# Optimization experiments

Measured on AMD Instinct MI355X. Metric: run time of the kernel, lower is better.

Reference implementation:

```python
import jax, jax.numpy as jnp
import numpy as np


def conv1x1(x, w, b):
    # x: [B,C,H,W], w: [O,C], b: [O]
    return jnp.einsum('bchw,oc->bohw', x, w) + b[None, :, None, None]


def dwconv(x, w):
    # depthwise conv, x: [B,C,H,W], w: [C,1,k,k], SAME padding (k odd, pad=k//2)
    return jax.lax.conv_general_dilated(
        x, w, window_strides=(1, 1), padding='SAME',
        dimension_numbers=('NCHW', 'OIHW', 'NCHW'),
        feature_group_count=x.shape[1])


def setup_inputs() -> dict:
    key = jax.random.key(0)
    ks = jax.random.split(key, 14)
    B, C, H, W = 16, 256, 64, 64
    OC = C // 16  # scale=16 -> 16
    WSCALE = 0.05
    r = lambda k, shape: jax.random.normal(k, shape, dtype=jnp.float32) * WSCALE
    return {
        'x': jax.random.normal(ks[0], (B, C, H, W), dtype=jnp.float32),
        'conv_w': r(ks[1], (C + 4, C)),           # 1x1 conv -> ctx (C) + gates (3+1)
        'conv_b': r(ks[2], (C + 4,)),
        'fw3': r(ks[3], (C, 1, 3, 3)),            # depthwise focal kernels
        'fw5': r(ks[4], (C, 1, 5, 5)),
        'fw7': r(ks[5], (C, 1, 7, 7)),
        'key_w': r(ks[6], (1, C)),                # Conv_key 1x1
        'key_b': r(ks[7], (1,)),
        'v1_w': r(ks[8], (OC, C)),                # Conv_value first 1x1
        'v1_b': r(ks[9], (OC,)),
        'ln_w': jnp.ones((OC,), dtype=jnp.float32),
        'ln_b': jnp.zeros((OC,), dtype=jnp.float32),
        'v2_w': r(ks[10], (C, OC)),               # Conv_value second 1x1
        'v2_b': r(ks[11], (C,)),
    }


def reference(x, conv_w, conv_b, fw3, fw5, fw7, key_w, key_b,
              v1_w, v1_b, ln_w, ln_b, v2_w, v2_b):
    B, C, H, W = x.shape
    # _contextAggregation
    t = conv1x1(x, conv_w, conv_b)          # [B, C+4, H, W]
    ctx, gates = t[:, :C], t[:, C:]         # [B,C,H,W], [B,4,H,W]
    ctx_all = jnp.zeros_like(ctx)
    for l, fw in enumerate((fw3, fw5, fw7)):
        ctx = jax.nn.gelu(dwconv(ctx, fw), approximate=False)  # torch GELU = exact erf
        ctx_all = ctx_all + ctx * gates[:, l:l + 1]
    ctx_global = jnp.mean(ctx, axis=(2, 3), keepdims=True)     # AdaptiveAvgPool2d(1)
    ctx_all = ctx_all + ctx_global * gates[:, 3:4]
    # GC-style channel attention: softmax over spatial positions
    k = conv1x1(ctx_all, key_w, key_b).reshape(B, H * W)       # [B, HW]
    k = jax.nn.softmax(k, axis=1)
    q = ctx_all.reshape(B, C, H * W)
    qk = jnp.einsum('bcn,bn->bc', q, k)[:, :, None, None]      # [B,C,1,1]
    # Conv_value: 1x1 -> LayerNorm([OC,1,1]) -> ReLU -> 1x1
    v = conv1x1(qk, v1_w, v1_b)                                # [B,OC,1,1]
    mu = jnp.mean(v, axis=(1, 2, 3), keepdims=True)
    var = jnp.var(v, axis=(1, 2, 3), keepdims=True)
    v = (v - mu) * jax.lax.rsqrt(var + 1e-5)
    v = v * ln_w[None, :, None, None] + ln_b[None, :, None, None]
    v = jax.nn.relu(v)
    v = conv1x1(v, v2_w, v2_b)                                 # [B,C,1,1]
    return ctx_all + v
```

## Files before the change

### kernel.cpp

```cpp
#include <hip/hip_runtime.h>

#define DEVFN __device__ __forceinline__

constexpr int B  = 16;
constexpr int C  = 256;
constexpr int N  = 64 * 64;
constexpr int O1 = C + 4;

typedef __attribute__((ext_vector_type(8)))  short bf16x8;
typedef __attribute__((ext_vector_type(4)))  short bf16x4;
typedef __attribute__((ext_vector_type(16))) float f32x16;
typedef __attribute__((ext_vector_type(2)))  _Float16 h2;
typedef unsigned short ushort_t;
typedef unsigned int   uint32;

DEVFN short f2bf(float f){
  union { float f; unsigned u; } p; p.f = f;
  unsigned r = p.u + 0x7fffu + ((p.u >> 16) & 1u);
  return (short)(r >> 16);
}
DEVFN unsigned pack2(float lo, float hi){
  return (unsigned)(ushort_t)f2bf(lo) | ((unsigned)(ushort_t)f2bf(hi) << 16);
}
DEVFN float lo2f(unsigned u){ union{unsigned u; float f;} p; p.u = u << 16; return p.f; }
DEVFN float hi2f(unsigned u){ union{unsigned u; float f;} p; p.u = u & 0xffff0000u; return p.f; }
DEVFN float bf2f(ushort_t s){ union{unsigned u; float f;} p; p.u = (unsigned)s << 16; return p.f; }

DEVFN float gelu_fast(float x){
  float s = x * x;
  float t = x * fmaf(s, 0.1029432f, 2.3022082f);
  float e = __builtin_amdgcn_exp2f(-t);
  return x * __builtin_amdgcn_rcpf(1.0f + e);
}

DEVFN float fdot2f(uint32 a, uint32 b, float c){
#if __has_builtin(__builtin_amdgcn_fdot2)
  return __builtin_amdgcn_fdot2(__builtin_bit_cast(h2, a),
                                __builtin_bit_cast(h2, b), c, false);
#else
  h2 ha = __builtin_bit_cast(h2, a), hb = __builtin_bit_cast(h2, b);
  return fmaf((float)ha.x, (float)hb.x, fmaf((float)ha.y, (float)hb.y, c));
#endif
}

DEVFN uint32 pkh(float a, float b){
  _Float16 ha = (_Float16)a, hb = (_Float16)b;
  return (uint32)__builtin_bit_cast(ushort_t, ha) |
         ((uint32)__builtin_bit_cast(ushort_t, hb) << 16);
}

__global__ __launch_bounds__(256)
void k_wbf(const float* __restrict__ w, ushort_t* __restrict__ wbf,
           const float* __restrict__ fw3, const float* __restrict__ fw5,
           const float* __restrict__ fw7, uint32* __restrict__ w3p,
           uint32* __restrict__ w5p, uint32* __restrict__ w7p){
  if(blockIdx.x == 320){
    const int c = threadIdx.x;
    #pragma unroll
    for(int ky = 0; ky < 3; ky++){
      const float* wr = fw3 + c * 9 + ky * 3;
      w3p[c * 6 + ky * 2 + 0] = pkh(wr[0], wr[1]);
      w3p[c * 6 + ky * 2 + 1] = pkh(wr[2], 0.f);
    }
    #pragma unroll
    for(int ky = 0; ky < 5; ky++){
      const float* wr = fw5 + c * 25 + ky * 5;
      w5p[c * 15 + ky * 3 + 0] = pkh(wr[0], wr[1]);
      w5p[c * 15 + ky * 3 + 1] = pkh(wr[2], wr[3]);
      w5p[c * 15 + ky * 3 + 2] = pkh(wr[4], 0.f);
    }
    #pragma unroll
    for(int ky = 0; ky < 7; ky++){
      const float* wr = fw7 + c * 49 + ky * 7;
      w7p[c * 28 + ky * 4 + 0] = pkh(wr[0], wr[1]);
      w7p[c * 28 + ky * 4 + 1] = pkh(wr[2], wr[3]);
      w7p[c * 28 + ky * 4 + 2] = pkh(wr[4], wr[5]);
      w7p[c * 28 + ky * 4 + 3] = pkh(wr[6], 0.f);
    }
    return;
  }
  int idx = blockIdx.x * 256 + threadIdx.x;
  int o = idx >> 8, cc = idx & 255;
  wbf[idx] = (o < O1) ? (ushort_t)f2bf(w[o * 256 + cc]) : (ushort_t)0;
}

__global__ __launch_bounds__(256, 3)
void k_conv1_mfma(const float* __restrict__ x, const ushort_t* __restrict__ wbf,
                  const float* __restrict__ bias, ushort_t* __restrict__ ctxb,
                  float* __restrict__ gates){
  __shared__ __align__(16) short wlds[8 * 320 * 8];
  __shared__ __align__(16) short xlds[8 * 64 * 8];
  __shared__ float sbias[320];
  const int tid  = threadIdx.x;
  const int wave = tid >> 6;
  const int lane = tid & 63;
  const int l31  = lane & 31;
  const int lhi  = lane >> 5;
  const int pg0  = blockIdx.x * 64;
  const int b    = pg0 >> 12;
  const int n0   = pg0 & 4095;
  const int nwv  = (wave & 1) * 32;
  const int mrow = wave >> 1;

  sbias[tid] = bias[tid];
  if(tid < 64) sbias[256 + tid] = (256 + tid < O1) ? bias[256 + tid] : 0.f;

  const float* xpb = x + (size_t)b * C * N + n0;

  f32x16 acc[5];
  #pragma unroll
  for(int t = 0; t < 5; t++)
    #pragma unroll
    for(int r = 0; r < 16; r++) acc[t][r] = 0.f;

  float xf[2][8];

  auto pfX = [&](int kc){
    #pragma unroll
    for(int p = 0; p < 2; p++){
      const int idx = p * 256 + tid;
      const int kg = idx >> 6, n = idx & 63;
      const float* xp = xpb + (size_t)(kc + kg * 8) * N + n;
      #pragma unroll
      for(int j = 0; j < 8; j++) xf[p][j] = xp[(size_t)j * N];
    }
  };
  auto stX = [&](){
    #pragma unroll
    for(int p = 0; p < 2; p++){
      const int idx = p * 256 + tid;
      const int kg = idx >> 6, n = idx & 63;
      uint4 v;
      v.x = pack2(xf[p][0], xf[p][1]); v.y = pack2(xf[p][2], xf[p][3]);
      v.z = pack2(xf[p][4], xf[p][5]); v.w = pack2(xf[p][6], xf[p][7]);
      *(uint4*)&xlds[(kg * 64 + n) * 8] = v;
    }
  };
  auto stW = [&](int kc){
    #pragma unroll
    for(int q = 0; q < 10; q++){
      const int pidx = q * 256 + tid;
      const int kg = pidx / 320;
      const int m  = pidx - kg * 320;
      uint4 v = *(const uint4*)(wbf + (size_t)m * 256 + kc + kg * 8);
      *(uint4*)&wlds[(kg * 320 + m) * 8] = v;
    }
  };
  auto mfmaC = [&](){
    #pragma unroll
    for(int ks = 0; ks < 4; ks++){
      const int kg = ks * 2 + lhi;
      bf16x8 bfr = *(const bf16x8*)&xlds[(kg * 64 + nwv + l31) * 8];
      #pragma unroll
      for(int t = 0; t < 5; t++){
        const int m0 = (mrow + 2 * t) * 32;
        bf16x8 af = *(const bf16x8*)&wlds[(kg * 320 + m0 + l31) * 8];
        acc[t] = __builtin_amdgcn_mfma_f32_32x32x16_bf16(af, bfr, acc[t], 0, 0, 0);
      }
    }
  };

  stW(0); pfX(0); stX();
  __syncthreads();
  pfX(64);
  mfmaC();
  __syncthreads();
  stW(64); stX();
  __syncthreads();
  pfX(128);
  mfmaC();
  __syncthreads();
  stW(128); stX();
  __syncthreads();
  pfX(192);
  mfmaC();
  __syncthreads();
  stW(192); stX();
  __syncthreads();
  mfmaC();

  const int n = n0 + nwv + l31;
  #pragma unroll
  for(int t = 0; t < 5; t++){
    const int mt = (mrow + 2 * t) * 32;
    #pragma unroll
    for(int r = 0; r < 16; r++){
      const int row = (r & 3) + 8 * (r >> 2) + 4 * lhi;
      const int o = mt + row;
      if(o >= O1) continue;
      const float v = acc[t][r] + sbias[o];
      if(o < 256){
        _Float16 hv = (_Float16)v;
        ctxb[((size_t)(b * 256 + o)) * N + n] = __builtin_bit_cast(ushort_t, hv);
      } else {
        gates[((size_t)(b * 4 + (o - 256))) * N + n] = v;
      }
    }
  }
}

constexpr int SSTR = 72;

template<int K>
DEVFN void dw_stage_dot(const short* src, const uint32* __restrict__ wp,
                        int h, int w0, float* val){
  constexpr int R = K / 2;
  constexpr int PAIRS = (K + 2) / 2;
  float acc[8];
  #pragma unroll
  for(int i = 0; i < 8; i++) acc[i] = 0.f;
  #pragma unroll
  for(int ky = 0; ky < K; ky++){
    uint32 wk[PAIRS];
    #pragma unroll
    for(int t = 0; t < PAIRS; t++) wk[t] = wp[ky * PAIRS + t];
    const int r = h + ky - R;
    if((unsigned)r < 64u){
      const short* rp = &src[r * SSTR + w0];
      uint4 a0 = *(const uint4*)rp;
      uint4 a1 = *(const uint4*)(rp + 8);
      uint32 P[8] = {a0.x, a0.y, a0.z, a0.w, a1.x, a1.y, a1.z, a1.w};
      uint32 S[7];
      #pragma unroll
      for(int j = 0; j < 7; j++)
        S[j] = __builtin_amdgcn_alignbit(P[j + 1], P[j], 16);
      #pragma unroll
      for(int i = 0; i < 8; i++){
        int j0, useP;
        if      (K == 7){ useP =  (i & 1); j0 = (i + 1) >> 1; }
        else if (K == 5){ useP = !(i & 1); j0 = (i >> 1) + 1; }
        else            { useP =  (i & 1); j0 = (i >> 1) + ((i & 1) ? 2 : 1); }
        #pragma unroll
        for(int t = 0; t < PAIRS; t++){
          const uint32 a = useP ? P[j0 + t] : S[j0 + t];
          acc[i] = fdot2f(a, wk[t], acc[i]);
        }
      }
    }
  }
  #pragma unroll
  for(int i = 0; i < 8; i++) val[i] = gelu_fast(acc[i]);
}

DEVFN void store_row_h(short* dst, int h, int w0, const float* val){
  uint32 o0 = __builtin_bit_cast(uint32, __builtin_amdgcn_cvt_pkrtz(val[0], val[1]));
  uint32 o1 = __builtin_bit_cast(uint32, __builtin_amdgcn_cvt_pkrtz(val[2], val[3]));
  uint32 o2 = __builtin_bit_cast(uint32, __builtin_amdgcn_cvt_pkrtz(val[4], val[5]));
  uint32 o3 = __builtin_bit_cast(uint32, __builtin_amdgcn_cvt_pkrtz(val[6], val[7]));
  uint2 t0; t0.x = o0; t0.y = o1;
  uint2 t1; t1.x = o2; t1.y = o3;
  *(uint2*)&dst[h * SSTR + w0 + 4] = t0;
  *(uint2*)&dst[h * SSTR + w0 + 8] = t1;
}

__global__ __launch_bounds__(512, 8)
void k_dwchain(ushort_t* __restrict__ ctxb, const uint32* __restrict__ w3p,
               const uint32* __restrict__ w5p, const uint32* __restrict__ w7p,
               const float* __restrict__ gates){
  __shared__ __align__(16) short bufA[64 * SSTR];
  __shared__ __align__(16) short bufB[64 * SSTR];
  __shared__ float wred[8];
  const int tid = threadIdx.x;
  const int plane = blockIdx.x;
  const int b = plane >> 8;
  const int c = plane & 255;
  const int h  = tid >> 3;
  const int w0 = (tid & 7) * 8;
  const int nbase = h * 64 + w0;

  if(tid < 64){
    bf16x4 z = {0, 0, 0, 0};
    *(bf16x4*)&bufA[tid * SSTR] = z;  *(bf16x4*)&bufA[tid * SSTR + 68] = z;
    *(bf16x4*)&bufB[tid * SSTR] = z;  *(bf16x4*)&bufB[tid * SSTR + 68] = z;
  }
  {
    const uint4 iv = *(const uint4*)((const short*)ctxb + (size_t)plane * N + tid * 8);
    uint2 t0; t0.x = iv.x; t0.y = iv.y;
    uint2 t1; t1.x = iv.z; t1.y = iv.w;
    *(uint2*)&bufA[h * SSTR + w0 + 4] = t0;
    *(uint2*)&bufA[h * SSTR + w0 + 8] = t1;
  }
  __syncthreads();

  float ctxp[8];
  #pragma unroll
  for(int i = 0; i < 8; i++) ctxp[i] = 0.f;
  float val[8];

  dw_stage_dot<3>(bufA, w3p + c * 6, h, w0, val);
  {
    const float* gp = gates + ((size_t)(b * 4 + 0)) * N + nbase;
    float4 ga = *(const float4*)gp, gb = *(const float4*)(gp + 4);
    ctxp[0] = fmaf(val[0], ga.x, ctxp[0]); ctxp[1] = fmaf(val[1], ga.y, ctxp[1]);
    ctxp[2] = fmaf(val[2], ga.z, ctxp[2]); ctxp[3] = fmaf(val[3], ga.w, ctxp[3]);
    ctxp[4] = fmaf(val[4], gb.x, ctxp[4]); ctxp[5] = fmaf(val[5], gb.y, ctxp[5]);
    ctxp[6] = fmaf(val[6], gb.z, ctxp[6]); ctxp[7] = fmaf(val[7], gb.w, ctxp[7]);
    store_row_h(bufB, h, w0, val);
  }
  __syncthreads();

  dw_stage_dot<5>(bufB, w5p + c * 15, h, w0, val);
  {
    const float* gp = gates + ((size_t)(b * 4 + 1)) * N + nbase;
    float4 ga = *(const float4*)gp, gb = *(const float4*)(gp + 4);
    ctxp[0] = fmaf(val[0], ga.x, ctxp[0]); ctxp[1] = fmaf(val[1], ga.y, ctxp[1]);
    ctxp[2] = fmaf(val[2], ga.z, ctxp[2]); ctxp[3] = fmaf(val[3], ga.w, ctxp[3]);
    ctxp[4] = fmaf(val[4], gb.x, ctxp[4]); ctxp[5] = fmaf(val[5], gb.y, ctxp[5]);
    ctxp[6] = fmaf(val[6], gb.z, ctxp[6]); ctxp[7] = fmaf(val[7], gb.w, ctxp[7]);
    store_row_h(bufA, h, w0, val);
  }
  __syncthreads();

  dw_stage_dot<7>(bufA, w7p + c * 28, h, w0, val);
  float lsum = 0.f;
  {
    const float* gp = gates + ((size_t)(b * 4 + 2)) * N + nbase;
    float4 ga = *(const float4*)gp, gb = *(const float4*)(gp + 4);
    ctxp[0] = fmaf(val[0], ga.x, ctxp[0]); ctxp[1] = fmaf(val[1], ga.y, ctxp[1]);
    ctxp[2] = fmaf(val[2], ga.z, ctxp[2]); ctxp[3] = fmaf(val[3], ga.w, ctxp[3]);
    ctxp[4] = fmaf(val[4], gb.x, ctxp[4]); ctxp[5] = fmaf(val[5], gb.y, ctxp[5]);
    ctxp[6] = fmaf(val[6], gb.z, ctxp[6]); ctxp[7] = fmaf(val[7], gb.w, ctxp[7]);
    #pragma unroll
    for(int i = 0; i < 8; i++) lsum += val[i];
  }
  #pragma unroll
  for(int off = 32; off > 0; off >>= 1) lsum += __shfl_xor(lsum, off, 64);
  if((tid & 63) == 0) wred[tid >> 6] = lsum;
  __syncthreads();
  float mean = 0.f;
  #pragma unroll
  for(int i = 0; i < 8; i++) mean += wred[i];
  mean *= (1.0f / 4096.0f);

  {
    const float* gp = gates + ((size_t)(b * 4 + 3)) * N + nbase;
    float4 ga = *(const float4*)gp, gb = *(const float4*)(gp + 4);
    bf16x8 ov;
    ov[0] = f2bf(fmaf(mean, ga.x, ctxp[0])); ov[1] = f2bf(fmaf(mean, ga.y, ctxp[1]));
    ov[2] = f2bf(fmaf(mean, ga.z, ctxp[2])); ov[3] = f2bf(fmaf(mean, ga.w, ctxp[3]));
    ov[4] = f2bf(fmaf(mean, gb.x, ctxp[4])); ov[5] = f2bf(fmaf(mean, gb.y, ctxp[5]));
    ov[6] = f2bf(fmaf(mean, gb.z, ctxp[6])); ov[7] = f2bf(fmaf(mean, gb.w, ctxp[7]));
    *(bf16x8*)((short*)ctxb + (size_t)plane * N + nbase) = ov;
  }
}

__global__ __launch_bounds__(256)
void k_logits(const ushort_t* __restrict__ P, const float* __restrict__ key_w,
              const float* __restrict__ key_b, float* __restrict__ logits){
  __shared__ float kw[256];
  __shared__ float part[512];
  int tid = threadIdx.x;
  kw[tid] = key_w[tid];
  __syncthreads();
  int b  = blockIdx.x >> 5;
  int n0 = (blockIdx.x & 31) * 128;
  int cpart = tid >> 6, pxp = tid & 63;
  const ushort_t* pp = P + ((size_t)(b * 256 + cpart * 64)) * N + n0 + pxp * 2;
  float a0 = 0.f, a1 = 0.f;
  #pragma unroll 8
  for(int c = 0; c < 64; c++){
    unsigned u = *(const unsigned*)(pp + (size_t)c * N);
    float kwv = kw[cpart * 64 + c];
    a0 = fmaf(lo2f(u), kwv, a0);
    a1 = fmaf(hi2f(u), kwv, a1);
  }
  part[cpart * 128 + pxp * 2]     = a0;
  part[cpart * 128 + pxp * 2 + 1] = a1;
  __syncthreads();
  if(tid < 128){
    float l = part[tid] + part[128 + tid] + part[256 + tid] + part[384 + tid];
    logits[b * N + n0 + tid] = l + key_b[0];
  }
}

__global__ __launch_bounds__(1024)
void k_softmax(float* __restrict__ kbuf){
  __shared__ float wred[16];
  int b = blockIdx.x, tid = threadIdx.x;
  const int wave = tid >> 6, lane = tid & 63;
  float v[4];
  float m = -1e30f;
  #pragma unroll
  for(int i = 0; i < 4; i++){
    v[i] = kbuf[b * N + tid + i * 1024];
    m = fmaxf(m, v[i]);
  }
  #pragma unroll
  for(int off = 32; off > 0; off >>= 1) m = fmaxf(m, __shfl_xor(m, off, 64));
  if(lane == 0) wred[wave] = m;
  __syncthreads();
  float mm = -1e30f;
  #pragma unroll
  for(int i = 0; i < 16; i++) mm = fmaxf(mm, wred[i]);
  __syncthreads();
  float s = 0.f;
  #pragma unroll
  for(int i = 0; i < 4; i++){ v[i] = __expf(v[i] - mm); s += v[i]; }
  #pragma unroll
  for(int off = 32; off > 0; off >>= 1) s += __shfl_xor(s, off, 64);
  if(lane == 0) wred[wave] = s;
  __syncthreads();
  float tot = 0.f;
  #pragma unroll
  for(int i = 0; i < 16; i++) tot += wred[i];
  float inv = 1.0f / tot;
  #pragma unroll
  for(int i = 0; i < 4; i++)
    kbuf[b * N + tid + i * 1024] = v[i] * inv;
}

__global__ __launch_bounds__(256)
void k_qk(const ushort_t* __restrict__ P, const float* __restrict__ kbuf,
          float* __restrict__ qk){
  __shared__ float red[256];
  int plane = blockIdx.x, tid = threadIdx.x;
  int b = plane >> 8;
  const unsigned* pp = (const unsigned*)(P + (size_t)plane * N);
  const float2* kp = (const float2*)(kbuf + b * N);
  float acc = 0.f;
  #pragma unroll
  for(int i = 0; i < 8; i++){
    int idx = tid + i * 256;
    unsigned u = pp[idx];
    float2 kk = kp[idx];
    acc = fmaf(lo2f(u), kk.x, acc);
    acc = fmaf(hi2f(u), kk.y, acc);
  }
  red[tid] = acc; __syncthreads();
  for(int s = 128; s > 0; s >>= 1){
    if(tid < s) red[tid] += red[tid + s];
    __syncthreads();
  }
  if(tid == 0) qk[plane] = red[0];
}

__global__ __launch_bounds__(256)
void k_v(const float* __restrict__ qk, const float* __restrict__ v1w,
         const float* __restrict__ v1b, const float* __restrict__ lnw,
         const float* __restrict__ lnb, const float* __restrict__ v2w,
         const float* __restrict__ v2b, float* __restrict__ vout){
  int b = blockIdx.x, tid = threadIdx.x;
  __shared__ float qs[256];
  __shared__ float part[256];
  __shared__ float v1s[16];
  __shared__ float vr[16];
  __shared__ float stats[2];
  qs[tid] = qk[b * 256 + tid];
  __syncthreads();
  int oc = tid >> 4, ln = tid & 15;
  float p = 0.f;
  #pragma unroll
  for(int j = 0; j < 16; j++){
    int cc = ln + j * 16;
    p = fmaf(v1w[oc * 256 + cc], qs[cc], p);
  }
  part[tid] = p;
  __syncthreads();
  if(tid < 16){
    float s = v1b[tid];
    for(int j = 0; j < 16; j++) s += part[tid * 16 + j];
    v1s[tid] = s;
  }
  __syncthreads();
  if(tid == 0){
    float mu = 0.f;
    for(int i = 0; i < 16; i++) mu += v1s[i];
    mu *= (1.f / 16.f);
    float var = 0.f;
    for(int i = 0; i < 16; i++){ float d = v1s[i] - mu; var += d * d; }
    var *= (1.f / 16.f);
    stats[0] = mu; stats[1] = rsqrtf(var + 1e-5f);
  }
  __syncthreads();
  if(tid < 16){
    float vv = (v1s[tid] - stats[0]) * stats[1] * lnw[tid] + lnb[tid];
    vr[tid] = fmaxf(vv, 0.f);
  }
  __syncthreads();
  float o = v2b[tid];
  #pragma unroll
  for(int j = 0; j < 16; j++) o = fmaf(v2w[tid * 16 + j], vr[j], o);
  vout[b * 256 + tid] = o;
}

__global__ __launch_bounds__(256)
void k_final(float* __restrict__ out, const ushort_t* __restrict__ ctxb,
             const float* __restrict__ vout){
  int idx8 = blockIdx.x * 256 + threadIdx.x;
  int plane = idx8 >> 9;
  int off = (idx8 & 511) * 8;
  bf16x8 v = *(const bf16x8*)((const short*)ctxb + (size_t)plane * N + off);
  float vv = vout[plane];
  float4 o0, o1;
  o0.x = bf2f((ushort_t)v[0]) + vv; o0.y = bf2f((ushort_t)v[1]) + vv;
  o0.z = bf2f((ushort_t)v[2]) + vv; o0.w = bf2f((ushort_t)v[3]) + vv;
  o1.x = bf2f((ushort_t)v[4]) + vv; o1.y = bf2f((ushort_t)v[5]) + vv;
  o1.z = bf2f((ushort_t)v[6]) + vv; o1.w = bf2f((ushort_t)v[7]) + vv;
  float* op = out + (size_t)plane * N + off;
  *(float4*)op = o0;
  *(float4*)(op + 4) = o1;
}

extern "C" void kernel_launch(void* const* d_in, const int* in_sizes, int n_in,
                              void* d_out, int out_size, void* d_ws, size_t ws_size,
                              hipStream_t stream){
  const float* x      = (const float*)d_in[0];
  const float* conv_w = (const float*)d_in[1];
  const float* conv_b = (const float*)d_in[2];
  const float* fw3    = (const float*)d_in[3];
  const float* fw5    = (const float*)d_in[4];
  const float* fw7    = (const float*)d_in[5];
  const float* key_w  = (const float*)d_in[6];
  const float* key_b  = (const float*)d_in[7];
  const float* v1_w   = (const float*)d_in[8];
  const float* v1_b   = (const float*)d_in[9];
  const float* ln_w   = (const float*)d_in[10];
  const float* ln_b   = (const float*)d_in[11];
  const float* v2_w   = (const float*)d_in[12];
  const float* v2_b   = (const float*)d_in[13];
  float* out = (float*)d_out;

  const size_t PL = (size_t)B * C * N;
  char* p = (char*)d_ws;
  ushort_t* ctxb = (ushort_t*)p;  p += PL * sizeof(ushort_t);
  float* gates   = (float*)p;     p += (size_t)B * 4 * N * sizeof(float);
  float* kbuf    = (float*)p;     p += (size_t)B * N * sizeof(float);
  float* qkb     = (float*)p;     p += (size_t)B * C * sizeof(float);
  float* vout    = (float*)p;     p += (size_t)B * C * sizeof(float);
  ushort_t* wbf  = (ushort_t*)p;  p += (size_t)320 * 256 * sizeof(ushort_t);
  uint32* w3p    = (uint32*)p;    p += (size_t)256 * 6 * sizeof(uint32);
  uint32* w5p    = (uint32*)p;    p += (size_t)256 * 15 * sizeof(uint32);
  uint32* w7p    = (uint32*)p;

  k_wbf<<<321, 256, 0, stream>>>(conv_w, wbf, fw3, fw5, fw7, w3p, w5p, w7p);
  k_conv1_mfma<<<1024, 256, 0, stream>>>(x, wbf, conv_b, ctxb, gates);
  k_dwchain<<<B * C, 512, 0, stream>>>(ctxb, w3p, w5p, w7p, gates);
  k_logits<<<512, 256, 0, stream>>>(ctxb, key_w, key_b, kbuf);
  k_softmax<<<B, 1024, 0, stream>>>(kbuf);
  k_qk<<<B * C, 256, 0, stream>>>(ctxb, kbuf, qkb);
  k_v<<<B, 256, 0, stream>>>(qkb, v1_w, v1_b, ln_w, ln_b, v2_w, v2_b, vout);
  k_final<<<8192, 256, 0, stream>>>(out, ctxb, vout);
}
```

Before: 270.8 us.

## Split gate channels out of MFMA conv1x1 and widen block to 512 threads

The 1x1 conv kernel no longer pads the 260 output rows to 320 for MFMA. It computes only the 256 ctx channels with MFMA, and the 4 gate channels are computed by scalar FMAs from the staged x tile and fp32 gate weights held in shared memory. The block grows to 8 waves, each owning 32 output rows by 64 pixels. Weight loads are prefetched into registers before the barrier, overlapping them with compute. This removes about 20% of wasted MFMA work and weight traffic, at the cost of extra scalar ALU and LDS reads for the gates on half the threads, and the launch bounds of 512 threads with 6 blocks may force heavy register limits.

```diff
diff --git a/kernel.cpp b/kernel.cpp
--- a/kernel.cpp
+++ b/kernel.cpp
@@ -84,119 +84,136 @@
   wbf[idx] = (o < O1) ? (ushort_t)f2bf(w[o * 256 + cc]) : (ushort_t)0;
 }
 
-__global__ __launch_bounds__(256, 3)
+__global__ __launch_bounds__(512, 6)
 void k_conv1_mfma(const float* __restrict__ x, const ushort_t* __restrict__ wbf,
-                  const float* __restrict__ bias, ushort_t* __restrict__ ctxb,
-                  float* __restrict__ gates){
-  __shared__ __align__(16) short wlds[8 * 320 * 8];
+                  const float* __restrict__ conv_w, const float* __restrict__ bias,
+                  ushort_t* __restrict__ ctxb, float* __restrict__ gates){
+  __shared__ __align__(16) short wlds[8 * 256 * 8];
   __shared__ __align__(16) short xlds[8 * 64 * 8];
-  __shared__ float sbias[320];
+  __shared__ float sgw[4 * 256];
+  __shared__ float sbias[256];
   const int tid  = threadIdx.x;
   const int wave = tid >> 6;
   const int lane = tid & 63;
   const int l31  = lane & 31;
   const int lhi  = lane >> 5;
-  const int pg0  = blockIdx.x * 64;
-  const int b    = pg0 >> 12;
-  const int n0   = pg0 & 4095;
-  const int nwv  = (wave & 1) * 32;
-  const int mrow = wave >> 1;
-
-  sbias[tid] = bias[tid];
-  if(tid < 64) sbias[256 + tid] = (256 + tid < O1) ? bias[256 + tid] : 0.f;
+  const int pg   = blockIdx.x;
+  const int b    = pg >> 6;
+  const int n0   = (pg & 63) * 64;
+
+  #pragma unroll
+  for(int i = 0; i < 2; i++) sgw[i * 512 + tid] = conv_w[256 * 256 + i * 512 + tid];
+  if(tid < 256) sbias[tid] = bias[tid];
+  const int gidx = tid >> 6;
+  const int gn   = tid & 63;
+  float gbias = (tid < 256) ? bias[256 + gidx] : 0.f;
+  float gacc = 0.f;
 
   const float* xpb = x + (size_t)b * C * N + n0;
 
-  f32x16 acc[5];
-  #pragma unroll
-  for(int t = 0; t < 5; t++)
+  f32x16 acc[2];
+  #pragma unroll
+  for(int t = 0; t < 2; t++)
     #pragma unroll
     for(int r = 0; r < 16; r++) acc[t][r] = 0.f;
 
-  float xf[2][8];
+  float xf[8];
+  uint4 wf[4];
 
   auto pfX = [&](int kc){
-    #pragma unroll
-    for(int p = 0; p < 2; p++){
-      const int idx = p * 256 + tid;
-      const int kg = idx >> 6, n = idx & 63;
-      const float* xp = xpb + (size_t)(kc + kg * 8) * N + n;
-      #pragma unroll
-      for(int j = 0; j < 8; j++) xf[p][j] = xp[(size_t)j * N];
-    }
+    const int kg = wave, n = lane;
+    const float* xp = xpb + (size_t)(kc + kg * 8) * N + n;
+    #pragma unroll
+    for(int j = 0; j < 8; j++) xf[j] = xp[(size_t)j * N];
   };
   auto stX = [&](){
-    #pragma unroll
-    for(int p = 0; p < 2; p++){
-      const int idx = p * 256 + tid;
-      const int kg = idx >> 6, n = idx & 63;
-      uint4 v;
-      v.x = pack2(xf[p][0], xf[p][1]); v.y = pack2(xf[p][2], xf[p][3]);
-      v.z = pack2(xf[p][4], xf[p][5]); v.w = pack2(xf[p][6], xf[p][7]);
-      *(uint4*)&xlds[(kg * 64 + n) * 8] = v;
-    }
+    const int kg = wave, n = lane;
+    uint4 v;
+    v.x = pack2(xf[0], xf[1]); v.y = pack2(xf[2], xf[3]);
+    v.z = pack2(xf[4], xf[5]); v.w = pack2(xf[6], xf[7]);
+    *(uint4*)&xlds[(kg * 64 + n) * 8] = v;
   };
-  auto stW = [&](int kc){
-    #pragma unroll
-    for(int q = 0; q < 10; q++){
-      const int pidx = q * 256 + tid;
-      const int kg = pidx / 320;
-      const int m  = pidx - kg * 320;
-      uint4 v = *(const uint4*)(wbf + (size_t)m * 256 + kc + kg * 8);
-      *(uint4*)&wlds[(kg * 320 + m) * 8] = v;
+  auto pfW = [&](int kc){
+    #pragma unroll
+    for(int q = 0; q < 4; q++){
+      const int pidx = q * 512 + tid;
+      const int kg = pidx >> 8;
+      const int m  = pidx & 255;
+      wf[q] = *(const uint4*)(wbf + (size_t)m * 256 + kc + kg * 8);
+    }
+  };
+  auto stW = [&](){
+    #pragma unroll
+    for(int q = 0; q < 4; q++){
+      const int pidx = q * 512 + tid;
+      const int kg = pidx >> 8;
+      const int m  = pidx & 255;
+      *(uint4*)&wlds[(kg * 256 + m) * 8] = wf[q];
     }
   };
   auto mfmaC = [&](){
     #pragma unroll
     for(int ks = 0; ks < 4; ks++){
       const int kg = ks * 2 + lhi;
-      bf16x8 bfr = *(const bf16x8*)&xlds[(kg * 64 + nwv + l31) * 8];
+      bf16x8 af = *(const bf16x8*)&wlds[(kg * 256 + wave * 32 + l31) * 8];
+      bf16x8 b0 = *(const bf16x8*)&xlds[(kg * 64 + l31) * 8];
+      bf16x8 b1 = *(const bf16x8*)&xlds[(kg * 64 + 32 + l31) * 8];
+      acc[0] = __builtin_amdgcn_mfma_f32_32x32x16_bf16(af, b0, acc[0], 0, 0, 0);
+      acc[1] = __builtin_amdgcn_mfma_f32_32x32x16_bf16(af, b1, acc[1], 0, 0, 0);
+    }
+  };
+  auto gateC = [&](int kc){
+    if(tid < 256){
+      float a = gacc;
       #pragma unroll
-      for(int t = 0; t < 5; t++){
-        const int m0 = (mrow + 2 * t) * 32;
-        bf16x8 af = *(const bf16x8*)&wlds[(kg * 320 + m0 + l31) * 8];
-        acc[t] = __builtin_amdgcn_mfma_f32_32x32x16_bf16(af, bfr, acc[t], 0, 0, 0);
+      for(int kg = 0; kg < 8; kg++){
+        bf16x8 xv = *(const bf16x8*)&xlds[(kg * 64 + gn) * 8];
+        const float* gw = &sgw[gidx * 256 + kc + kg * 8];
+        #pragma unroll
+        for(int j = 0; j < 4; j++){
+          unsigned u = ((const unsigned*)&xv)[j];
+          a = fmaf(lo2f(u), gw[2 * j], a);
+          a = fmaf(hi2f(u), gw[2 * j + 1], a);
+        }
       }
+      gacc = a;
     }
   };
 
-  stW(0); pfX(0); stX();
-  __syncthreads();
-  pfX(64);
-  mfmaC();
-  __syncthreads();
-  stW(64); stX();
-  __syncthreads();
-  pfX(128);
-  mfmaC();
-  __syncthreads();
-  stW(128); stX();
-  __syncthreads();
-  pfX(192);
-  mfmaC();
-  __syncthreads();
-  stW(192); stX();
-  __syncthreads();
-  mfmaC();
-
-  const int n = n0 + nwv + l31;
-  #pragma unroll
-  for(int t = 0; t < 5; t++){
-    const int mt = (mrow + 2 * t) * 32;
+  pfX(0); pfW(0);
+  stX(); stW();
+  __syncthreads();
+  pfX(64); pfW(64);
+  mfmaC(); gateC(0);
+  __syncthreads();
+  stX(); stW();
+  __syncthreads();
+  pfX(128); pfW(128);
+  mfmaC(); gateC(64);
+  __syncthreads();
+  stX(); stW();
+  __syncthreads();
+  pfX(192); pfW(192);
+  mfmaC(); gateC(128);
+  __syncthreads();
+  stX(); stW();
+  __syncthreads();
+  mfmaC(); gateC(192);
+
+  #pragma unroll
+  for(int nt = 0; nt < 2; nt++){
+    const int n = n0 + nt * 32 + l31;
     #pragma unroll
     for(int r = 0; r < 16; r++){
       const int row = (r & 3) + 8 * (r >> 2) + 4 * lhi;
-      const int o = mt + row;
-      if(o >= O1) continue;
-      const float v = acc[t][r] + sbias[o];
-      if(o < 256){
-        _Float16 hv = (_Float16)v;
-        ctxb[((size_t)(b * 256 + o)) * N + n] = __builtin_bit_cast(ushort_t, hv);
-      } else {
-        gates[((size_t)(b * 4 + (o - 256))) * N + n] = v;
-      }
-    }
-  }
+      const int o = wave * 32 + row;
+      const float v = acc[nt][r] + sbias[o];
+      _Float16 hv = (_Float16)v;
+      ctxb[((size_t)(b * 256 + o)) * N + n] = __builtin_bit_cast(ushort_t, hv);
+    }
+  }
+  if(tid < 256)
+    gates[((size_t)(b * 4 + gidx)) * N + n0 + gn] = gacc + gbias;
 }
 
 constexpr int SSTR = 72;
@@ -533,7 +550,7 @@
   uint32* w7p    = (uint32*)p;
 
   k_wbf<<<321, 256, 0, stream>>>(conv_w, wbf, fw3, fw5, fw7, w3p, w5p, w7p);
-  k_conv1_mfma<<<1024, 256, 0, stream>>>(x, wbf, conv_b, ctxb, gates);
+  k_conv1_mfma<<<1024, 512, 0, stream>>>(x, wbf, conv_w, conv_b, ctxb, gates);
   k_dwchain<<<B * C, 512, 0, stream>>>(ctxb, w3p, w5p, w7p, gates);
   k_logits<<<512, 256, 0, stream>>>(ctxb, key_w, key_b, kbuf);
   k_softmax<<<B, 1024, 0, stream>>>(kbuf);
```

New measurement: 320.2 us. +18.3%, slower.
